# Kernel optimization log

Measured on AMD Instinct MI355X. Metric: run time of the kernel, lower is better.

Reference implementation:

```python
import jax, jax.numpy as jnp
import numpy as np

N, D, C, T, E = 8192, 512, 4, 8, 32768
H = D  # hidden_nf == input_nf == output_nf (required by the module's own shapes)


def _silu(x):
    return x * jax.nn.sigmoid(x)


def _lin(x, W, b):
    # torch Linear convention: W is [out, in]
    y = jnp.einsum('...i,oi->...o', x, W)
    return y + b


def setup_inputs() -> dict:
    key = jax.random.key(0)
    ks = jax.random.split(key, 20)
    s = 0.05  # keep activations in a sane range through stacked SiLU MLPs
    return {
        'h': jax.random.normal(ks[0], (N, D), jnp.float32),
        'coord': jax.random.normal(ks[1], (N, C, 3), jnp.float32),
        'edge_attr': jax.random.normal(ks[2], (T, E, 1), jnp.float32),
        'edge_index': jax.random.randint(ks[3], (T, 2, E), 0, N),
        'mW1': jax.random.normal(ks[4], (H, 2 * D + C * C + 1), jnp.float32) * s,
        'mb1': jnp.zeros((H,), jnp.float32),
        'mW2': jax.random.normal(ks[5], (H, H), jnp.float32) * s,
        'mb2': jnp.zeros((H,), jnp.float32),
        'nW1': jax.random.normal(ks[6], (H, H + D), jnp.float32) * s,
        'nb1': jnp.zeros((H,), jnp.float32),
        'nW2': jax.random.normal(ks[7], (D, H), jnp.float32) * s,
        'nb2': jnp.zeros((D,), jnp.float32),
        'eW1': jax.random.normal(ks[8], (H, H + 1 + H), jnp.float32) * s,
        'eb1': jnp.zeros((H,), jnp.float32),
        'eW2': jax.random.normal(ks[9], (1, H), jnp.float32) * s,
        'eb2': jnp.zeros((1,), jnp.float32),
        'relW': jax.random.normal(ks[10], (T, D, H), jnp.float32) * s,
        'cW1': jax.random.normal(ks[11], (T, H, H), jnp.float32) * s,
        'cb1': jnp.zeros((T, H), jnp.float32),
        'cW2': jax.random.normal(ks[12], (T, C, H), jnp.float32) * (s * 0.001),  # xavier gain=0.001
    }


def reference(h, coord, edge_attr, edge_index, mW1, mb1, mW2, mb2,
              nW1, nb1, nW2, nb2, eW1, eb1, eW2, eb2, relW, cW1, cb1, cW2):
    n, d = h.shape
    t, _, e = edge_index.shape
    c = coord.shape[1]
    row = edge_index[:, 0]  # [T,E]
    col = edge_index[:, 1]

    # coord2radial (per type, vectorized over type axis)
    cd = coord[row] - coord[col]                              # [T,E,C,3]
    radial = jnp.einsum('teca,teda->tecd', cd, cd)            # [T,E,C,C]
    # F.normalize(radial, dim=0): L2-normalize across the edge axis of each type
    nrm = jnp.sqrt(jnp.sum(radial * radial, axis=1, keepdims=True))
    radial = radial / jnp.maximum(nrm, 1e-12)

    # message_model (dropout = identity in eval)
    feat = jnp.concatenate([h[row], h[col], radial.reshape(t, e, c * c), edge_attr], axis=-1)
    msg = _silu(_lin(_silu(_lin(feat, mW1, mb1)), mW2, mb2))  # [T,E,H]

    # node_model: per-type segment_sum -> per-type relation linear -> sum
    seg = jax.vmap(lambda dta, ids: jax.ops.segment_sum(dta, ids, num_segments=n))(msg, row)  # [T,N,H]
    agg = jnp.einsum('tnh,tdh->nd', seg, relW)                # sum over types
    h_new = h + _lin(_silu(_lin(jnp.concatenate([h, agg], axis=-1), nW1, nb1)), nW2, nb2)

    # coord_model: per-type coord MLP weights, segment-mean over all types' edges
    hid = _silu(jnp.einsum('teh,tgh->teg', msg, cW1) + cb1[:, None, :])
    w = jnp.einsum('teg,tcg->tec', hid, cW2)                  # [T,E,C]
    trans = cd * w[..., None]                                 # [T,E,C,3]
    rows_flat = row.reshape(-1)
    sumv = jax.ops.segment_sum(trans.reshape(t * e, c, 3), rows_flat, num_segments=n)
    cnt = jax.ops.segment_sum(jnp.ones((t * e,), trans.dtype), rows_flat, num_segments=n)
    x_new = coord + sumv / jnp.maximum(cnt, 1.0)[:, None, None]

    # edge_model (note: forward passes edge_attr here, not the messages)
    ef = jnp.concatenate([h_new[row], edge_attr, h_new[col]], axis=-1)  # [T,E,H+1+H]
    m = _lin(_silu(_lin(ef, eW1, eb1)), eW2, eb2)             # [T,E,1]

    return (h_new, x_new, m)
```

## Files before the change

### kernel.cpp

```cpp
#include <hip/hip_runtime.h>
#include <cstdint>

#define NN 8192
#define DD 512
#define CC 4
#define TT 8
#define EE 32768
#define TE (TT*EE)

typedef __attribute__((ext_vector_type(8))) short short8v;
typedef __attribute__((ext_vector_type(4))) float f32x4;
typedef unsigned int uint;

constexpr int FLAG_SILU = 1, FLAG_RES = 2, FLAG_WEPI = 4, FLAG_BIAS_T = 8;

__device__ __forceinline__ float silu_f(float x) { return x / (1.f + __expf(-x)); }

__device__ __forceinline__ unsigned short f2bf(float f) {
  uint u = __builtin_bit_cast(uint, f);
  u += 0x7fffu + ((u >> 16) & 1u);
  return (unsigned short)(u >> 16);
}
__device__ __forceinline__ float bf2f(unsigned short b) {
  uint u = ((uint)b) << 16;
  return __builtin_bit_cast(float, u);
}
__device__ __forceinline__ float bflo(uint u) { return __builtin_bit_cast(float, u << 16); }
__device__ __forceinline__ float bfhi(uint u) { return __builtin_bit_cast(float, u & 0xffff0000u); }
__device__ __forceinline__ uint packbf(float a, float b) {
  return (uint)f2bf(a) | ((uint)f2bf(b) << 16);
}

__device__ __forceinline__ float wave_sum(float v) {
#pragma unroll
  for (int off = 32; off; off >>= 1) v += __shfl_xor(v, off);
  return v;
}

__device__ __forceinline__ void gload16(const void* g, void* l) {
  __builtin_amdgcn_global_load_lds(
      (const __attribute__((address_space(1))) void*)g,
      (__attribute__((address_space(3))) void*)l, 16, 0, 0);
}

__device__ __forceinline__ int xcd_swz(int i, int nwg) {
  return (i & 7) * (nwg >> 3) + (i >> 3);
}

struct AgDirect { const unsigned short* p; int K;
  __device__ const void* ptr(int m, int k, int) const { return p + (size_t)m * K + k; } };

struct AgHcat { const unsigned short* hb; const unsigned short* ab;
  __device__ const void* ptr(int m, int k, int) const {
    return (k < 512) ? (const void*)(hb + ((size_t)m << 9) + k)
                     : (const void*)(ab + ((size_t)m << 9) + (k - 512)); } };

struct AgSegG { const unsigned short* seg;
  __device__ const void* ptr(int m, int k, int) const {
    return seg + (((size_t)(k >> 9) * NN + m) << 9) + (k & 511); } };

struct BgDirect { const unsigned short* p; int K;
  __device__ const void* ptr(int o, int k, int) const { return p + (size_t)o * K + k; } };

struct BgRelG { const unsigned short* w;
  __device__ const void* ptr(int o, int k, int) const {
    return w + (((size_t)(k >> 9) * 512 + o) << 9) + (k & 511); } };

struct BgPerT { const unsigned short* w;
  __device__ const void* ptr(int o, int k, int tt) const {
    return w + (((size_t)tt << 18) + ((size_t)o << 9)) + k; } };

template<class AG, class BG>
__global__ __launch_bounds__(256)
void mgemm_k(AG ag, BG bg, int K, int tbase, int lognx,
             const float* __restrict__ bias, const float* __restrict__ res,
             float* __restrict__ outF, unsigned short* __restrict__ outB, int ldo, int flags,
             const float* __restrict__ cw2, float* __restrict__ wpart, int wstride)
{
  __shared__ __align__(16) unsigned short SM[128 * 136];
  unsigned short* As = SM;
  unsigned short* Bs = SM + 128 * 64;
  const int nwg = gridDim.x;
  const int swz = xcd_swz(blockIdx.x, nwg);
  const int xb = swz & ((1 << lognx) - 1), yb = swz >> lognx;
  const int m0 = yb * 128, o0 = xb * 128;
  const int tt = tbase + (m0 >> 15);
  const int tid = threadIdx.x, wave = tid >> 6, lane = tid & 63;
  const int wr = (wave >> 1) * 64, wc = (wave & 1) * 64;
  const int rs = lane >> 3, sl = lane & 7;

  f32x4 acc[4][4];
#pragma unroll
  for (int i = 0; i < 4; ++i)
#pragma unroll
    for (int j = 0; j < 4; ++j) acc[i][j] = (f32x4)0.f;

  for (int k0 = 0; k0 < K; k0 += 64) {
#pragma unroll
    for (int i = 0; i < 4; ++i) {
      int r = i * 32 + wave * 8 + rs;
      int slot = sl ^ (r & 7);
      gload16(ag.ptr(m0 + r, k0 + slot * 8, tt), &As[(i * 32 + wave * 8) * 64]);
    }
#pragma unroll
    for (int i = 0; i < 4; ++i) {
      int r = i * 32 + wave * 8 + rs;
      int slot = sl ^ (r & 7);
      gload16(bg.ptr(o0 + r, k0 + slot * 8, tt), &Bs[(i * 32 + wave * 8) * 64]);
    }
    __syncthreads();

    short8v a[4][2], b[4][2];
#pragma unroll
    for (int mi = 0; mi < 4; ++mi)
#pragma unroll
      for (int s = 0; s < 2; ++s) {
        int row = wr + mi * 16 + (lane & 15);
        int slot = (s * 4 + (lane >> 4)) ^ (row & 7);
        a[mi][s] = *(const short8v*)&As[row * 64 + slot * 8];
      }
#pragma unroll
    for (int ni = 0; ni < 4; ++ni)
#pragma unroll
      for (int s = 0; s < 2; ++s) {
        int row = wc + ni * 16 + (lane & 15);
        int slot = (s * 4 + (lane >> 4)) ^ (row & 7);
        b[ni][s] = *(const short8v*)&Bs[row * 64 + slot * 8];
      }
#pragma unroll
    for (int s = 0; s < 2; ++s)
#pragma unroll
      for (int mi = 0; mi < 4; ++mi)
#pragma unroll
        for (int ni = 0; ni < 4; ++ni)
          acc[mi][ni] = __builtin_amdgcn_mfma_f32_16x16x32_bf16(a[mi][s], b[ni][s], acc[mi][ni], 0, 0, 0);
    __syncthreads();
  }

  const int r4 = (lane >> 4) * 4, cl = lane & 15;
  if (flags & FLAG_WEPI) {
    const int slice = xb * 2 + (wave & 1);
    const float* cw2t = cw2 + tt * 2048;
    const float* bt = bias + tt * 512;
#pragma unroll
    for (int mi = 0; mi < 4; ++mi) {
      float sc[4][4];
#pragma unroll
      for (int rg = 0; rg < 4; ++rg)
#pragma unroll
        for (int c = 0; c < 4; ++c) sc[rg][c] = 0.f;
#pragma unroll
      for (int ni = 0; ni < 4; ++ni) {
        int col = o0 + wc + ni * 16 + cl;
        float c0 = cw2t[col], c1 = cw2t[512 + col], c2 = cw2t[1024 + col], c3 = cw2t[1536 + col];
        float bb = bt[col];
#pragma unroll
        for (int rg = 0; rg < 4; ++rg) {
          float v = silu_f(acc[mi][ni][rg] + bb);
          sc[rg][0] += v * c0; sc[rg][1] += v * c1; sc[rg][2] += v * c2; sc[rg][3] += v * c3;
        }
      }
#pragma unroll
      for (int rg = 0; rg < 4; ++rg)
#pragma unroll
        for (int c = 0; c < 4; ++c) {
          float s = sc[rg][c];
          s += __shfl_xor(s, 1); s += __shfl_xor(s, 2);
          s += __shfl_xor(s, 4); s += __shfl_xor(s, 8);
          sc[rg][c] = s;
        }
      if (cl == 0) {
        int p = m0 + wr + mi * 16 + r4;
#pragma unroll
        for (int rg = 0; rg < 4; ++rg) {
          float4 o = make_float4(sc[rg][0], sc[rg][1], sc[rg][2], sc[rg][3]);
          *(float4*)&wpart[(((size_t)slice * wstride) + p + rg) * 4] = o;
        }
      }
    }
    return;
  }
  if (outB && !outF) {
    unsigned short* Ep = SM;
#pragma unroll
    for (int mi = 0; mi < 4; ++mi)
#pragma unroll
      for (int ni = 0; ni < 4; ++ni)
#pragma unroll
        for (int rg = 0; rg < 4; ++rg) {
          int row = wr + mi * 16 + r4 + rg;
          int col = wc + ni * 16 + cl;
          float v = acc[mi][ni][rg];
          if (bias) v += (flags & FLAG_BIAS_T) ? bias[tt * 512 + o0 + col] : bias[o0 + col];
          if (flags & FLAG_SILU) v = silu_f(v);
          Ep[row * 136 + col] = f2bf(v);
        }
    __syncthreads();
#pragma unroll
    for (int p = 0; p < 8; ++p) {
      int idx = p * 256 + tid;
      int row = idx >> 4, ch = idx & 15;
      short8v vv = *(const short8v*)&Ep[row * 136 + ch * 8];
      *(short8v*)(outB + (size_t)(m0 + row) * ldo + o0 + ch * 8) = vv;
    }
    return;
  }
#pragma unroll
  for (int mi = 0; mi < 4; ++mi)
#pragma unroll
    for (int ni = 0; ni < 4; ++ni)
#pragma unroll
      for (int rg = 0; rg < 4; ++rg) {
        int row = m0 + wr + mi * 16 + r4 + rg;
        int col = o0 + wc + ni * 16 + cl;
        float v = acc[mi][ni][rg];
        if (bias) v += (flags & FLAG_BIAS_T) ? bias[tt * 512 + col] : bias[col];
        if (flags & FLAG_SILU) v = silu_f(v);
        if (flags & FLAG_RES) v += res[(size_t)row * ldo + col];
        if (outF) outF[(size_t)row * ldo + col] = v;
        if (outB) outB[(size_t)row * ldo + col] = f2bf(v);
      }
}

__global__ __launch_bounds__(256)
void cvt_k(const float* __restrict__ in, unsigned short* __restrict__ out, int n) {
  int i = blockIdx.x * 256 + threadIdx.x;
  if (i < n) out[i] = f2bf(in[i]);
}

__global__ __launch_bounds__(256)
void slicew_k(const float* __restrict__ w, unsigned short* __restrict__ o, int Kin, int col0) {
  int i = blockIdx.x * 256 + threadIdx.x;
  int r = i >> 9, k = i & 511;
  o[i] = f2bf(w[(size_t)r * Kin + col0 + k]);
}

__global__ __launch_bounds__(256)
void tailw_k(const float* __restrict__ mW1, unsigned short* __restrict__ o) {
  int i = blockIdx.x * 256 + threadIdx.x;
  if (i >= 17 * 512) return;
  int j = i >> 9, c = i & 511;
  o[i] = f2bf(mW1[(size_t)c * 1041 + 1024 + j]);
}

__global__ __launch_bounds__(256)
void weaw_k(const float* __restrict__ eW1, float* __restrict__ wea) {
  int i = blockIdx.x * 256 + threadIdx.x;
  if (i < 512) wea[i] = eW1[(size_t)i * 1025 + 512];
}

__global__ __launch_bounds__(256)
void biasb_k(const float* __restrict__ mb1, const float* __restrict__ eb1,
             float* __restrict__ pqb, float* __restrict__ ggb) {
  int i = blockIdx.x * 256 + threadIdx.x;
  if (i < 1024) {
    pqb[i] = (i < 512) ? mb1[i] : 0.f;
    ggb[i] = (i < 512) ? eb1[i] : 0.f;
  }
}

__global__ __launch_bounds__(256)
void hist_k(const int* __restrict__ eidx, int* __restrict__ deg) {
  int id = blockIdx.x * 256 + threadIdx.x;
  int t = id >> 15, e = id & (EE - 1);
  atomicAdd(&deg[(t << 13) + eidx[(t << 16) + e]], 1);
}

__global__ __launch_bounds__(256)
void scan_k(const int* __restrict__ deg, int* __restrict__ off, int* __restrict__ cursor) {
  int t = blockIdx.x, tid = threadIdx.x;
  __shared__ int lds[256];
  int base = 0;
  for (int ch = 0; ch < 32; ++ch) {
    int i = ch * 256 + tid;
    int v = deg[(t << 13) + i];
    __syncthreads();
    lds[tid] = v;
    __syncthreads();
    for (int s = 1; s < 256; s <<= 1) {
      int x = (tid >= s) ? lds[tid - s] : 0;
      __syncthreads();
      if (tid >= s) lds[tid] += x;
      __syncthreads();
    }
    int excl = base + lds[tid] - v;
    off[(t << 13) + i] = excl;
    cursor[(t << 13) + i] = excl;
    base += lds[255];
  }
}

__global__ __launch_bounds__(256)
void scat_k(const int* __restrict__ eidx, const float* __restrict__ ea, int* __restrict__ cursor,
            int* __restrict__ order, int* __restrict__ rank,
            int* __restrict__ rowS, int* __restrict__ colS, float* __restrict__ eaS) {
  int id = blockIdx.x * 256 + threadIdx.x;
  int t = id >> 15, e = id & (EE - 1);
  int r = eidx[(t << 16) + e], c = eidx[(t << 16) + EE + e];
  int pos = atomicAdd(&cursor[(t << 13) + r], 1);
  size_t g = ((size_t)t << 15) + pos;
  order[g] = e; rank[id] = pos; rowS[g] = r; colS[g] = c; eaS[g] = ea[id];
}

__global__ __launch_bounds__(256)
void cdrad_k(const float* __restrict__ coord, const int* __restrict__ eidx,
             const int* __restrict__ rank,
             float* __restrict__ cd, float* __restrict__ radial, float* __restrict__ pnrm)
{
  int m = blockIdx.x * 256 + threadIdx.x;
  int t = m >> 15, e = m & (EE - 1);
  int r = eidx[(t << 16) + e], c = eidx[(t << 16) + EE + e];
  size_t s = ((size_t)t << 15) + rank[m];
  const float4* cv4 = (const float4*)coord;
  float4 A0 = cv4[r * 3], A1 = cv4[r * 3 + 1], A2 = cv4[r * 3 + 2];
  float4 B0 = cv4[c * 3], B1 = cv4[c * 3 + 1], B2 = cv4[c * 3 + 2];
  float d[12] = {A0.x-B0.x, A0.y-B0.y, A0.z-B0.z, A0.w-B0.w,
                 A1.x-B1.x, A1.y-B1.y, A1.z-B1.z, A1.w-B1.w,
                 A2.x-B2.x, A2.y-B2.y, A2.z-B2.z, A2.w-B2.w};
  float4* cdv = (float4*)cd;
  cdv[s*3+0] = make_float4(d[0],d[1],d[2],d[3]);
  cdv[s*3+1] = make_float4(d[4],d[5],d[6],d[7]);
  cdv[s*3+2] = make_float4(d[8],d[9],d[10],d[11]);
  float rad[16], sq[16];
#pragma unroll
  for (int ci = 0; ci < 4; ++ci)
#pragma unroll
    for (int di = 0; di < 4; ++di) {
      float v = d[ci*3]*d[di*3] + d[ci*3+1]*d[di*3+1] + d[ci*3+2]*d[di*3+2];
      rad[ci*4+di] = v; sq[ci*4+di] = v * v;
    }
  float4* rv = (float4*)radial;
#pragma unroll
  for (int i = 0; i < 4; ++i)
    rv[s*4+i] = make_float4(rad[i*4], rad[i*4+1], rad[i*4+2], rad[i*4+3]);
#pragma unroll
  for (int i = 0; i < 16; ++i) sq[i] = wave_sum(sq[i]);
  __shared__ float red[4][16];
  int wv = threadIdx.x >> 6, lane = threadIdx.x & 63;
  if (lane == 0) {
#pragma unroll
    for (int i = 0; i < 16; ++i) red[wv][i] = sq[i];
  }
  __syncthreads();
  if (threadIdx.x < 16)
    pnrm[blockIdx.x * 16 + threadIdx.x] =
        red[0][threadIdx.x] + red[1][threadIdx.x] + red[2][threadIdx.x] + red[3][threadIdx.x];
}

__global__ __launch_bounds__(128)
void nrmred_k(const float* __restrict__ pnrm, float* __restrict__ nrm) {
  int t = threadIdx.x >> 4, j = threadIdx.x & 15;
  float s = 0.f;
  for (int b = 0; b < 128; ++b) s += pnrm[((t * 128 + b) << 4) + j];
  nrm[(t << 4) + j] = s;
}

__global__ __launch_bounds__(256)
void tails_k(const float* __restrict__ radial, const float* __restrict__ nrm,
             const float* __restrict__ eaS, unsigned short* __restrict__ tailm)
{
  int m = blockIdx.x * 256 + threadIdx.x;
  int t = m >> 15;
  unsigned short tmp[24];
#pragma unroll
  for (int j = 0; j < 16; ++j) {
    float r = radial[(size_t)m * 16 + j] / fmaxf(sqrtf(nrm[(t << 4) + j]), 1e-12f);
    tmp[j] = f2bf(r);
  }
  tmp[16] = f2bf(eaS[m]);
#pragma unroll
  for (int j = 17; j < 24; ++j) tmp[j] = 0;
  uint4* dst = (uint4*)(tailm + (size_t)m * 24);
  dst[0] = ((const uint4*)tmp)[0];
  dst[1] = ((const uint4*)tmp)[1];
  dst[2] = ((const uint4*)tmp)[2];
}

__global__ __launch_bounds__(256)
void msg1f_k(const unsigned short* __restrict__ PQ, const unsigned short* __restrict__ Wt,
             const unsigned short* __restrict__ tailm_g,
             const int* __restrict__ rowS_g, const int* __restrict__ colS_g,
             unsigned short* __restrict__ out)
{
  int tid = threadIdx.x;
  int e0 = xcd_swz(blockIdx.x, gridDim.x) * 16;
  uint wreg[17];
#pragma unroll
  for (int j = 0; j < 17; ++j) wreg[j] = *(const uint*)(Wt + j * 512 + tid * 2);
  for (int i = 0; i < 16; ++i) {
    int p = e0 + i;
    int r = rowS_g[p], c = colS_g[p];
    uint pv = *(const uint*)(PQ + ((size_t)r << 10) + tid * 2);
    uint qv = *(const uint*)(PQ + ((size_t)c << 10) + 512 + tid * 2);
    uint4 t0 = *(const uint4*)(tailm_g + (size_t)p * 24);
    uint4 t1 = *(const uint4*)(tailm_g + (size_t)p * 24 + 8);
    uint  t2 = *(const uint*)(tailm_g + (size_t)p * 24 + 16);
    float tl[17] = {bflo(t0.x), bfhi(t0.x), bflo(t0.y), bfhi(t0.y),
                    bflo(t0.z), bfhi(t0.z), bflo(t0.w), bfhi(t0.w),
                    bflo(t1.x), bfhi(t1.x), bflo(t1.y), bfhi(t1.y),
                    bflo(t1.z), bfhi(t1.z), bflo(t1.w), bfhi(t1.w),
                    bflo(t2)};
    float s0 = bflo(pv) + bflo(qv);
    float s1 = bfhi(pv) + bfhi(qv);
#pragma unroll
    for (int j = 0; j < 17; ++j) {
      s0 += tl[j] * bflo(wreg[j]); s1 += tl[j] * bfhi(wreg[j]);
    }
    *(uint*)(out + ((size_t)p << 9) + tid * 2) = packbf(silu_f(s0), silu_f(s1));
  }
}

__global__ __launch_bounds__(256)
void gsum_k(const unsigned short* __restrict__ msg, const int* __restrict__ offb,
            const int* __restrict__ deg, int tbase, unsigned short* __restrict__ segt)
{
  int l = xcd_swz(blockIdx.x, gridDim.x);
  int tloc = l >> 13, n = l & (NN - 1), tid = threadIdx.x;
  int t = tbase + tloc;
  int start = offb[(t << 13) + n], d = deg[(t << 13) + n];
  float s0 = 0.f, s1 = 0.f;
  const unsigned short* base = msg + (((size_t)tloc << 15) << 9);
  for (int j = 0; j < d; ++j) {
    uint v = *(const uint*)(base + ((size_t)(start + j) << 9) + tid * 2);
    s0 += bflo(v); s1 += bfhi(v);
  }
  *(uint*)(segt + (((size_t)tloc * NN + n) << 9) + tid * 2) = packbf(s0, s1);
}

__global__ __launch_bounds__(256)
void wsum_k(const float* __restrict__ wpart, float* __restrict__ wsum_out, int wstride) {
  int id = xcd_swz(blockIdx.x, gridDim.x) * 256 + threadIdx.x;
  float4 a = (float4){0.f, 0.f, 0.f, 0.f};
#pragma unroll
  for (int s = 0; s < 8; ++s) {
    float4 v = *(const float4*)&wpart[(((size_t)s * wstride) + id) * 4];
    a.x += v.x; a.y += v.y; a.z += v.z; a.w += v.w;
  }
  *(float4*)&wsum_out[(size_t)id * 4] = a;
}

__global__ __launch_bounds__(256)
void trxn_k(const float* __restrict__ coord, const float* __restrict__ cd,
            const float* __restrict__ wsum, const int* __restrict__ offb,
            const int* __restrict__ deg, float* __restrict__ xout)
{
  int id = blockIdx.x * 256 + threadIdx.x;
  int n = id / 12, j = id - n * 12, ci = j / 3;
  float s = 0.f; int cnt = 0;
#pragma unroll
  for (int t = 0; t < 8; ++t) {
    int o = offb[(t << 13) + n], d = deg[(t << 13) + n];
    size_t p = ((size_t)t << 15) + o;
    for (int k = 0; k < d; ++k)
      s += cd[(p + k) * 12 + j] * wsum[(p + k) * 4 + ci];
    cnt += d;
  }
  xout[id] = coord[id] + s / fmaxf((float)cnt, 1.f);
}

__global__ __launch_bounds__(256)
void mout_k(const unsigned short* __restrict__ GG,
            const float* __restrict__ eW2, const float* __restrict__ wea,
            const float* __restrict__ eb2, const float* __restrict__ eaS,
            const int* __restrict__ rowS, const int* __restrict__ colS,
            const int* __restrict__ order, float* __restrict__ out_m)
{
  int wid = blockIdx.x * 4 + (threadIdx.x >> 6);
  int lane = threadIdx.x & 63;
  int t = wid >> 15;
  int r = rowS[wid], c = colS[wid];
  float eav = eaS[wid];
  short8v gv  = *(const short8v*)(GG + ((size_t)r << 10) + lane * 8);
  short8v gcv = *(const short8v*)(GG + ((size_t)c << 10) + 512 + lane * 8);
  const float4* w4 = (const float4*)(eW2 + lane * 8);
  const float4* a4 = (const float4*)(wea + lane * 8);
  float4 w0 = w4[0], w1 = w4[1], a0 = a4[0], a1 = a4[1];
  float wv8[8] = {w0.x,w0.y,w0.z,w0.w,w1.x,w1.y,w1.z,w1.w};
  float av8[8] = {a0.x,a0.y,a0.z,a0.w,a1.x,a1.y,a1.z,a1.w};
  float s = 0.f;
#pragma unroll
  for (int j = 0; j < 8; ++j)
    s += wv8[j] * silu_f(bf2f((unsigned short)gv[j]) + bf2f((unsigned short)gcv[j]) + eav * av8[j]);
  s = wave_sum(s);
  if (lane == 0) out_m[((size_t)t << 15) + order[wid]] = s + eb2[0];
}

extern "C" void kernel_launch(void* const* d_in, const int* in_sizes, int n_in,
                              void* d_out, int out_size, void* d_ws, size_t ws_size,
                              hipStream_t stream)
{
  const float* h     = (const float*)d_in[0];
  const float* coord = (const float*)d_in[1];
  const float* ea    = (const float*)d_in[2];
  const int*   eidx  = (const int*)  d_in[3];
  const float* mW1   = (const float*)d_in[4];
  const float* mb1   = (const float*)d_in[5];
  const float* mW2   = (const float*)d_in[6];
  const float* mb2   = (const float*)d_in[7];
  const float* nW1   = (const float*)d_in[8];
  const float* nb1   = (const float*)d_in[9];
  const float* nW2   = (const float*)d_in[10];
  const float* nb2   = (const float*)d_in[11];
  const float* eW1   = (const float*)d_in[12];
  const float* eb1   = (const float*)d_in[13];
  const float* eW2   = (const float*)d_in[14];
  const float* eb2   = (const float*)d_in[15];
  const float* relW  = (const float*)d_in[16];
  const float* cW1   = (const float*)d_in[17];
  const float* cb1   = (const float*)d_in[18];
  const float* cW2   = (const float*)d_in[19];

  float* out   = (float*)d_out;
  float* out_h = out;
  float* out_x = out + (size_t)NN * DD;
  float* out_m = out_x + (size_t)NN * CC * 3;

  char* ws = (char*)d_ws;
  size_t off = 0;
  auto alloc = [&](size_t bytes) -> void* {
    void* p = ws + off; off += (bytes + 255) & ~(size_t)255; return p;
  };
  float* cd     = (float*)alloc((size_t)TE * 12 * 4);
  unsigned short* tailm = (unsigned short*)alloc((size_t)TE * 24 * 2);
  float* agg    = (float*)alloc((size_t)NN * 512 * 4);
  unsigned short* h_bf  = (unsigned short*)alloc((size_t)NN * 512 * 2);
  unsigned short* hn_bf = (unsigned short*)alloc((size_t)NN * 512 * 2);
  unsigned short* PQb   = (unsigned short*)alloc((size_t)NN * 1024 * 2);
  unsigned short* GGb   = PQb;
  unsigned short* mW1pq = (unsigned short*)alloc((size_t)1024 * 512 * 2);
  unsigned short* mW1t  = (unsigned short*)alloc((size_t)17 * 512 * 2);
  unsigned short* mW2b  = (unsigned short*)alloc((size_t)512 * 512 * 2);
  unsigned short* nW1b  = (unsigned short*)alloc((size_t)512 * 1024 * 2);
  unsigned short* nW2b  = (unsigned short*)alloc((size_t)512 * 512 * 2);
  unsigned short* eGc   = (unsigned short*)alloc((size_t)1024 * 512 * 2);
  float* weab   = (float*)alloc(512 * 4);
  float* pqbias = (float*)alloc(1024 * 4);
  float* ggbias = (float*)alloc(1024 * 4);
  unsigned short* relWb = (unsigned short*)alloc((size_t)TT * 512 * 512 * 2);
  unsigned short* cW1b  = (unsigned short*)alloc((size_t)TT * 512 * 512 * 2);
  int* deg     = (int*)alloc((size_t)TT * NN * 4);
  int* offb    = (int*)alloc((size_t)TT * NN * 4);
  int* cursor  = (int*)alloc((size_t)TT * NN * 4);
  int* order   = (int*)alloc((size_t)TE * 4);
  int* rank    = (int*)alloc((size_t)TE * 4);
  int* rowS    = (int*)alloc((size_t)TE * 4);
  int* colS    = (int*)alloc((size_t)TE * 4);
  float* eaS   = (float*)alloc((size_t)TE * 4);
  float* wsumb = (float*)alloc((size_t)TE * 4 * 4);
  float* pnrm  = (float*)alloc((size_t)(TE / 256) * 16 * 4);
  float* nrm   = (float*)alloc((size_t)TT * 16 * 4);

  const size_t perG = (size_t)EE * 512 * 2 * 2 + (size_t)NN * 512 * 2 + (size_t)8 * EE * 16;
  int G = 4;
  while (G > 1 && off + (size_t)G * perG + (1 << 20) > ws_size) G >>= 1;
  unsigned short* bufA = (unsigned short*)alloc((size_t)G * EE * 512 * 2);
  unsigned short* bufB = (unsigned short*)alloc((size_t)G * EE * 512 * 2);
  unsigned short* segt = (unsigned short*)alloc((size_t)G * NN * 512 * 2);
  float* wpart = (float*)alloc((size_t)8 * G * EE * 4 * 4);
  unsigned short* aggb = segt;
  float* radial = (float*)bufA;

  hipMemsetAsync(deg, 0, (size_t)TT * NN * 4, stream);
  hipMemsetAsync(agg, 0, (size_t)NN * 512 * 4, stream);

  auto cvt = [&](const float* in, unsigned short* o, int n) {
    cvt_k<<<(n + 255) / 256, 256, 0, stream>>>(in, o, n);
  };
  cvt(h,    h_bf,  NN * 512);
  cvt(mW2,  mW2b,  512 * 512);
  cvt(nW1,  nW1b,  512 * 1024);
  cvt(nW2,  nW2b,  512 * 512);
  cvt(relW, relWb, TT * 512 * 512);
  cvt(cW1,  cW1b,  TT * 512 * 512);
  slicew_k<<<1024, 256, 0, stream>>>(mW1, mW1pq, 1041, 0);
  slicew_k<<<1024, 256, 0, stream>>>(mW1, mW1pq + 512 * 512, 1041, 512);
  tailw_k<<<34, 256, 0, stream>>>(mW1, mW1t);
  slicew_k<<<1024, 256, 0, stream>>>(eW1, eGc, 1025, 0);
  slicew_k<<<1024, 256, 0, stream>>>(eW1, eGc + 512 * 512, 1025, 513);
  weaw_k<<<2, 256, 0, stream>>>(eW1, weab);
  biasb_k<<<4, 256, 0, stream>>>(mb1, eb1, pqbias, ggbias);

  hist_k<<<TE / 256, 256, 0, stream>>>(eidx, deg);
  scan_k<<<TT, 256, 0, stream>>>(deg, offb, cursor);
  scat_k<<<TE / 256, 256, 0, stream>>>(eidx, ea, cursor, order, rank, rowS, colS, eaS);
  cdrad_k<<<TE / 256, 256, 0, stream>>>(coord, eidx, rank, cd, radial, pnrm);
  nrmred_k<<<1, 128, 0, stream>>>(pnrm, nrm);
  tails_k<<<TE / 256, 256, 0, stream>>>(radial, nrm, eaS, tailm);

  mgemm_k<<<512, 256, 0, stream>>>(AgDirect{h_bf, 512}, BgDirect{mW1pq, 512}, 512, 0, 3,
      pqbias, nullptr, nullptr, PQb, 1024, 0, nullptr, nullptr, 0);

  for (int g = 0; g < TT / G; ++g) {
    const int tbase = g * G;
    const size_t gb = (size_t)tbase << 15;
    msg1f_k<<<(G * EE) / 16, 256, 0, stream>>>(PQb, mW1t, tailm + gb * 24,
        rowS + gb, colS + gb, bufA);
    mgemm_k<<<4 * (G * EE / 128), 256, 0, stream>>>(AgDirect{bufA, 512},
        BgDirect{mW2b, 512}, 512, tbase, 2,
        mb2, nullptr, nullptr, bufB, 512, FLAG_SILU, nullptr, nullptr, 0);
    gsum_k<<<G * NN, 256, 0, stream>>>(bufB, offb, deg, tbase, segt);
    mgemm_k<<<4 * (NN / 128), 256, 0, stream>>>(AgSegG{segt},
        BgRelG{relWb + ((size_t)tbase << 18)}, G * 512, 0, 2,
        nullptr, agg, agg, nullptr, 512, FLAG_RES, nullptr, nullptr, 0);
    mgemm_k<<<4 * (G * EE / 128), 256, 0, stream>>>(AgDirect{bufB, 512},
        BgPerT{cW1b}, 512, tbase, 2,
        cb1, nullptr, nullptr, nullptr, 512, FLAG_SILU | FLAG_WEPI | FLAG_BIAS_T,
        cW2, wpart, G * EE);
    wsum_k<<<(G * EE) / 256, 256, 0, stream>>>(wpart, wsumb + gb * 4, G * EE);
  }

  trxn_k<<<(NN * 12) / 256, 256, 0, stream>>>(coord, cd, wsumb, offb, deg, out_x);

  cvt(agg, aggb, NN * 512);
  mgemm_k<<<4 * (NN / 128), 256, 0, stream>>>(AgHcat{h_bf, aggb}, BgDirect{nW1b, 1024}, 1024, 0, 2,
      nb1, nullptr, nullptr, bufA, 512, FLAG_SILU, nullptr, nullptr, 0);
  mgemm_k<<<4 * (NN / 128), 256, 0, stream>>>(AgDirect{bufA, 512}, BgDirect{nW2b, 512}, 512, 0, 2,
      nb2, h, out_h, hn_bf, 512, FLAG_RES, nullptr, nullptr, 0);

  mgemm_k<<<512, 256, 0, stream>>>(AgDirect{hn_bf, 512}, BgDirect{eGc, 512}, 512, 0, 3,
      ggbias, nullptr, nullptr, GGb, 1024, 0, nullptr, nullptr, 0);
  mout_k<<<TE / 4, 256, 0, stream>>>(GGb, eW2, weab, eb2, eaS, rowS, colS, order, out_m);

  (void)in_sizes; (void)n_in; (void)out_size; (void)ws_size;
}
```

Before: 1.433 ms.

## Add 256-row 512-thread GEMM for edge MLPs, fuse converts and scatter kernels

```diff
diff --git a/kernel.cpp b/kernel.cpp
--- a/kernel.cpp
+++ b/kernel.cpp
@@ -74,14 +74,12 @@
 __global__ __launch_bounds__(256)
 void mgemm_k(AG ag, BG bg, int K, int tbase, int lognx,
              const float* __restrict__ bias, const float* __restrict__ res,
-             float* __restrict__ outF, unsigned short* __restrict__ outB, int ldo, int flags,
-             const float* __restrict__ cw2, float* __restrict__ wpart, int wstride)
+             float* __restrict__ outF, unsigned short* __restrict__ outB, int ldo, int flags)
 {
   __shared__ __align__(16) unsigned short SM[128 * 136];
   unsigned short* As = SM;
   unsigned short* Bs = SM + 128 * 64;
-  const int nwg = gridDim.x;
-  const int swz = xcd_swz(blockIdx.x, nwg);
+  const int swz = xcd_swz(blockIdx.x, gridDim.x);
   const int xb = swz & ((1 << lognx) - 1), yb = swz >> lognx;
   const int m0 = yb * 128, o0 = xb * 128;
   const int tt = tbase + (m0 >> 15);
@@ -109,7 +107,6 @@
       gload16(bg.ptr(o0 + r, k0 + slot * 8, tt), &Bs[(i * 32 + wave * 8) * 64]);
     }
     __syncthreads();
-
     short8v a[4][2], b[4][2];
 #pragma unroll
     for (int mi = 0; mi < 4; ++mi)
@@ -138,48 +135,6 @@
   }
 
   const int r4 = (lane >> 4) * 4, cl = lane & 15;
-  if (flags & FLAG_WEPI) {
-    const int slice = xb * 2 + (wave & 1);
-    const float* cw2t = cw2 + tt * 2048;
-    const float* bt = bias + tt * 512;
-#pragma unroll
-    for (int mi = 0; mi < 4; ++mi) {
-      float sc[4][4];
-#pragma unroll
-      for (int rg = 0; rg < 4; ++rg)
-#pragma unroll
-        for (int c = 0; c < 4; ++c) sc[rg][c] = 0.f;
-#pragma unroll
-      for (int ni = 0; ni < 4; ++ni) {
-        int col = o0 + wc + ni * 16 + cl;
-        float c0 = cw2t[col], c1 = cw2t[512 + col], c2 = cw2t[1024 + col], c3 = cw2t[1536 + col];
-        float bb = bt[col];
-#pragma unroll
-        for (int rg = 0; rg < 4; ++rg) {
-          float v = silu_f(acc[mi][ni][rg] + bb);
-          sc[rg][0] += v * c0; sc[rg][1] += v * c1; sc[rg][2] += v * c2; sc[rg][3] += v * c3;
-        }
-      }
-#pragma unroll
-      for (int rg = 0; rg < 4; ++rg)
-#pragma unroll
-        for (int c = 0; c < 4; ++c) {
-          float s = sc[rg][c];
-          s += __shfl_xor(s, 1); s += __shfl_xor(s, 2);
-          s += __shfl_xor(s, 4); s += __shfl_xor(s, 8);
-          sc[rg][c] = s;
-        }
-      if (cl == 0) {
-        int p = m0 + wr + mi * 16 + r4;
-#pragma unroll
-        for (int rg = 0; rg < 4; ++rg) {
-          float4 o = make_float4(sc[rg][0], sc[rg][1], sc[rg][2], sc[rg][3]);
-          *(float4*)&wpart[(((size_t)slice * wstride) + p + rg) * 4] = o;
-        }
-      }
-    }
-    return;
-  }
   if (outB && !outF) {
     unsigned short* Ep = SM;
 #pragma unroll
@@ -222,6 +177,164 @@
       }
 }
 
+template<class AG, class BG>
+__global__ __launch_bounds__(512)
+void mgemm2_k(AG ag, BG bg, int K, int tbase,
+              const float* __restrict__ bias,
+              unsigned short* __restrict__ outB, int flags,
+              const float* __restrict__ cw2, float* __restrict__ wpart, int wstride)
+{
+  __shared__ __align__(16) unsigned short SM[(256 + 128) * 64];
+  unsigned short* As = SM;
+  unsigned short* Bs = SM + 256 * 64;
+  const int swz = xcd_swz(blockIdx.x, gridDim.x);
+  const int xb = swz & 3, yb = swz >> 2;
+  const int m0 = yb * 256, o0 = xb * 128;
+  const int tt = tbase + (m0 >> 15);
+  const int tid = threadIdx.x, wave = tid >> 6, lane = tid & 63;
+  const int wr = (wave >> 1) * 64, wc = (wave & 1) * 64;
+  const int rs = lane >> 3, sl = lane & 7;
+
+  f32x4 acc[4][4];
+#pragma unroll
+  for (int i = 0; i < 4; ++i)
+#pragma unroll
+    for (int j = 0; j < 4; ++j) acc[i][j] = (f32x4)0.f;
+
+  for (int k0 = 0; k0 < K; k0 += 64) {
+#pragma unroll
+    for (int i = 0; i < 4; ++i) {
+      int r = i * 64 + wave * 8 + rs;
+      int slot = sl ^ (r & 7);
+      gload16(ag.ptr(m0 + r, k0 + slot * 8, tt), &As[(i * 64 + wave * 8) * 64]);
+    }
+#pragma unroll
+    for (int i = 0; i < 2; ++i) {
+      int r = i * 64 + wave * 8 + rs;
+      int slot = sl ^ (r & 7);
+      gload16(bg.ptr(o0 + r, k0 + slot * 8, tt), &Bs[(i * 64 + wave * 8) * 64]);
+    }
+    __syncthreads();
+    short8v a[4][2], b[4][2];
+#pragma unroll
+    for (int mi = 0; mi < 4; ++mi)
+#pragma unroll
+      for (int s = 0; s < 2; ++s) {
+        int row = wr + mi * 16 + (lane & 15);
+        int slot = (s * 4 + (lane >> 4)) ^ (row & 7);
+        a[mi][s] = *(const short8v*)&As[row * 64 + slot * 8];
+      }
+#pragma unroll
+    for (int ni = 0; ni < 4; ++ni)
+#pragma unroll
+      for (int s = 0; s < 2; ++s) {
+        int row = wc + ni * 16 + (lane & 15);
+        int slot = (s * 4 + (lane >> 4)) ^ (row & 7);
+        b[ni][s] = *(const short8v*)&Bs[row * 64 + slot * 8];
+      }
+#pragma unroll
+    for (int s = 0; s < 2; ++s)
+#pragma unroll
+      for (int mi = 0; mi < 4; ++mi)
+#pragma unroll
+        for (int ni = 0; ni < 4; ++ni)
+          acc[mi][ni] = __builtin_amdgcn_mfma_f32_16x16x32_bf16(a[mi][s], b[ni][s], acc[mi][ni], 0, 0, 0);
+    __syncthreads();
+  }
+
+  const int r4 = (lane >> 4) * 4, cl = lane & 15;
+  if (flags & FLAG_WEPI) {
+    const int slice = xb * 2 + (wave & 1);
+    const float* cw2t = cw2 + tt * 2048;
+    const float* bt = bias + tt * 512;
+#pragma unroll
+    for (int mi = 0; mi < 4; ++mi) {
+      float sc[4][4];
+#pragma unroll
+      for (int rg = 0; rg < 4; ++rg)
+#pragma unroll
+        for (int c = 0; c < 4; ++c) sc[rg][c] = 0.f;
+#pragma unroll
+      for (int ni = 0; ni < 4; ++ni) {
+        int col = o0 + wc + ni * 16 + cl;
+        float c0 = cw2t[col], c1 = cw2t[512 + col], c2 = cw2t[1024 + col], c3 = cw2t[1536 + col];
+        float bb = bt[col];
+#pragma unroll
+        for (int rg = 0; rg < 4; ++rg) {
+          float v = silu_f(acc[mi][ni][rg] + bb);
+          sc[rg][0] += v * c0; sc[rg][1] += v * c1; sc[rg][2] += v * c2; sc[rg][3] += v * c3;
+        }
+      }
+#pragma unroll
+      for (int rg = 0; rg < 4; ++rg)
+#pragma unroll
+        for (int c = 0; c < 4; ++c) {
+          float s = sc[rg][c];
+          s += __shfl_xor(s, 1); s += __shfl_xor(s, 2);
+          s += __shfl_xor(s, 4); s += __shfl_xor(s, 8);
+          sc[rg][c] = s;
+        }
+      if (cl == 0) {
+        int p = m0 + wr + mi * 16 + r4;
+#pragma unroll
+        for (int rg = 0; rg < 4; ++rg) {
+          float4 o = make_float4(sc[rg][0], sc[rg][1], sc[rg][2], sc[rg][3]);
+          *(float4*)&wpart[(((size_t)slice * wstride) + p + rg) * 4] = o;
+        }
+      }
+    }
+    return;
+  }
+  unsigned short* Ep = SM;
+#pragma unroll
+  for (int hh = 0; hh < 2; ++hh) {
+    if ((wr >> 7) == hh) {
+#pragma unroll
+      for (int mi = 0; mi < 4; ++mi)
+#pragma unroll
+        for (int ni = 0; ni < 4; ++ni)
+#pragma unroll
+          for (int rg = 0; rg < 4; ++rg) {
+            int row = (wr & 127) + mi * 16 + r4 + rg;
+            int col = wc + ni * 16 + cl;
+            float v = acc[mi][ni][rg];
+            v += bias[o0 + col];
+            if (flags & FLAG_SILU) v = silu_f(v);
+            Ep[row * 136 + col] = f2bf(v);
+          }
+    }
+    __syncthreads();
+#pragma unroll
+    for (int p = 0; p < 4; ++p) {
+      int idx = p * 512 + tid;
+      int row = idx >> 4, ch = idx & 15;
+      short8v vv = *(const short8v*)&Ep[row * 136 + ch * 8];
+      *(short8v*)(outB + (size_t)(m0 + hh * 128 + row) * 512 + o0 + ch * 8) = vv;
+    }
+    __syncthreads();
+  }
+}
+
+__global__ __launch_bounds__(256)
+void cvtall_k(const float* h, const float* mW2, const float* nW1, const float* nW2,
+              const float* relW, const float* cW1,
+              unsigned short* hb, unsigned short* mW2b, unsigned short* nW1b,
+              unsigned short* nW2b, unsigned short* relWb, unsigned short* cW1b)
+{
+  int i = blockIdx.x * 256 + threadIdx.x;
+  if (i < 4194304) { hb[i] = f2bf(h[i]); return; }
+  i -= 4194304;
+  if (i < 262144) { mW2b[i] = f2bf(mW2[i]); return; }
+  i -= 262144;
+  if (i < 524288) { nW1b[i] = f2bf(nW1[i]); return; }
+  i -= 524288;
+  if (i < 262144) { nW2b[i] = f2bf(nW2[i]); return; }
+  i -= 262144;
+  if (i < 2097152) { relWb[i] = f2bf(relW[i]); return; }
+  i -= 2097152;
+  cW1b[i] = f2bf(cW1[i]);
+}
+
 __global__ __launch_bounds__(256)
 void cvt_k(const float* __restrict__ in, unsigned short* __restrict__ out, int n) {
   int i = blockIdx.x * 256 + threadIdx.x;
@@ -291,26 +404,18 @@
 }
 
 __global__ __launch_bounds__(256)
-void scat_k(const int* __restrict__ eidx, const float* __restrict__ ea, int* __restrict__ cursor,
-            int* __restrict__ order, int* __restrict__ rank,
-            int* __restrict__ rowS, int* __restrict__ colS, float* __restrict__ eaS) {
-  int id = blockIdx.x * 256 + threadIdx.x;
-  int t = id >> 15, e = id & (EE - 1);
-  int r = eidx[(t << 16) + e], c = eidx[(t << 16) + EE + e];
-  int pos = atomicAdd(&cursor[(t << 13) + r], 1);
-  size_t g = ((size_t)t << 15) + pos;
-  order[g] = e; rank[id] = pos; rowS[g] = r; colS[g] = c; eaS[g] = ea[id];
-}
-
-__global__ __launch_bounds__(256)
-void cdrad_k(const float* __restrict__ coord, const int* __restrict__ eidx,
-             const int* __restrict__ rank,
-             float* __restrict__ cd, float* __restrict__ radial, float* __restrict__ pnrm)
+void scatcd_k(const int* __restrict__ eidx, const float* __restrict__ ea,
+              const float* __restrict__ coord, int* __restrict__ cursor,
+              int* __restrict__ order, int* __restrict__ rowS, int* __restrict__ colS,
+              float* __restrict__ eaS, float* __restrict__ cd,
+              float* __restrict__ radial, float* __restrict__ pnrm)
 {
   int m = blockIdx.x * 256 + threadIdx.x;
   int t = m >> 15, e = m & (EE - 1);
   int r = eidx[(t << 16) + e], c = eidx[(t << 16) + EE + e];
-  size_t s = ((size_t)t << 15) + rank[m];
+  int pos = atomicAdd(&cursor[(t << 13) + r], 1);
+  size_t s = ((size_t)t << 15) + pos;
+  order[s] = e; rowS[s] = r; colS[s] = c; eaS[s] = ea[m];
   const float4* cv4 = (const float4*)coord;
   float4 A0 = cv4[r * 3], A1 = cv4[r * 3 + 1], A2 = cv4[r * 3 + 2];
   float4 B0 = cv4[c * 3], B1 = cv4[c * 3 + 1], B2 = cv4[c * 3 + 2];
@@ -465,7 +570,7 @@
             const int* __restrict__ rowS, const int* __restrict__ colS,
             const int* __restrict__ order, float* __restrict__ out_m)
 {
-  int wid = blockIdx.x * 4 + (threadIdx.x >> 6);
+  int wid = xcd_swz(blockIdx.x, gridDim.x) * 4 + (threadIdx.x >> 6);
   int lane = threadIdx.x & 63;
   int t = wid >> 15;
   int r = rowS[wid], c = colS[wid];
@@ -542,7 +647,6 @@
   int* offb    = (int*)alloc((size_t)TT * NN * 4);
   int* cursor  = (int*)alloc((size_t)TT * NN * 4);
   int* order   = (int*)alloc((size_t)TE * 4);
-  int* rank    = (int*)alloc((size_t)TE * 4);
   int* rowS    = (int*)alloc((size_t)TE * 4);
   int* colS    = (int*)alloc((size_t)TE * 4);
   float* eaS   = (float*)alloc((size_t)TE * 4);
@@ -563,15 +667,8 @@
   hipMemsetAsync(deg, 0, (size_t)TT * NN * 4, stream);
   hipMemsetAsync(agg, 0, (size_t)NN * 512 * 4, stream);
 
-  auto cvt = [&](const float* in, unsigned short* o, int n) {
-    cvt_k<<<(n + 255) / 256, 256, 0, stream>>>(in, o, n);
-  };
-  cvt(h,    h_bf,  NN * 512);
-  cvt(mW2,  mW2b,  512 * 512);
-  cvt(nW1,  nW1b,  512 * 1024);
-  cvt(nW2,  nW2b,  512 * 512);
-  cvt(relW, relWb, TT * 512 * 512);
-  cvt(cW1,  cW1b,  TT * 512 * 512);
+  cvtall_k<<<9437184 / 256, 256, 0, stream>>>(h, mW2, nW1, nW2, relW, cW1,
+      h_bf, mW2b, nW1b, nW2b, relWb, cW1b);
   slicew_k<<<1024, 256, 0, stream>>>(mW1, mW1pq, 1041, 0);
   slicew_k<<<1024, 256, 0, stream>>>(mW1, mW1pq + 512 * 512, 1041, 512);
   tailw_k<<<34, 256, 0, stream>>>(mW1, mW1t);
@@ -582,43 +679,42 @@
 
   hist_k<<<TE / 256, 256, 0, stream>>>(eidx, deg);
   scan_k<<<TT, 256, 0, stream>>>(deg, offb, cursor);
-  scat_k<<<TE / 256, 256, 0, stream>>>(eidx, ea, cursor, order, rank, rowS, colS, eaS);
-  cdrad_k<<<TE / 256, 256, 0, stream>>>(coord, eidx, rank, cd, radial, pnrm);
+  scatcd_k<<<TE / 256, 256, 0, stream>>>(eidx, ea, coord, cursor,
+      order, rowS, colS, eaS, cd, radial, pnrm);
   nrmred_k<<<1, 128, 0, stream>>>(pnrm, nrm);
   tails_k<<<TE / 256, 256, 0, stream>>>(radial, nrm, eaS, tailm);
 
   mgemm_k<<<512, 256, 0, stream>>>(AgDirect{h_bf, 512}, BgDirect{mW1pq, 512}, 512, 0, 3,
-      pqbias, nullptr, nullptr, PQb, 1024, 0, nullptr, nullptr, 0);
+      pqbias, nullptr, nullptr, PQb, 1024, 0);
 
   for (int g = 0; g < TT / G; ++g) {
     const int tbase = g * G;
     const size_t gb = (size_t)tbase << 15;
     msg1f_k<<<(G * EE) / 16, 256, 0, stream>>>(PQb, mW1t, tailm + gb * 24,
         rowS + gb, colS + gb, bufA);
-    mgemm_k<<<4 * (G * EE / 128), 256, 0, stream>>>(AgDirect{bufA, 512},
-        BgDirect{mW2b, 512}, 512, tbase, 2,
-        mb2, nullptr, nullptr, bufB, 512, FLAG_SILU, nullptr, nullptr, 0);
+    mgemm2_k<<<4 * (G * EE / 256), 512, 0, stream>>>(AgDirect{bufA, 512},
+        BgDirect{mW2b, 512}, 512, tbase,
+        mb2, bufB, FLAG_SILU, nullptr, nullptr, 0);
     gsum_k<<<G * NN, 256, 0, stream>>>(bufB, offb, deg, tbase, segt);
     mgemm_k<<<4 * (NN / 128), 256, 0, stream>>>(AgSegG{segt},
         BgRelG{relWb + ((size_t)tbase << 18)}, G * 512, 0, 2,
-        nullptr, agg, agg, nullptr, 512, FLAG_RES, nullptr, nullptr, 0);
-    mgemm_k<<<4 * (G * EE / 128), 256, 0, stream>>>(AgDirect{bufB, 512},
-        BgPerT{cW1b}, 512, tbase, 2,
-        cb1, nullptr, nullptr, nullptr, 512, FLAG_SILU | FLAG_WEPI | FLAG_BIAS_T,
-        cW2, wpart, G * EE);
+        nullptr, agg, agg, nullptr, 512, FLAG_RES);
+    mgemm2_k<<<4 * (G * EE / 256), 512, 0, stream>>>(AgDirect{bufB, 512},
+        BgPerT{cW1b}, 512, tbase,
+        cb1, nullptr, FLAG_SILU | FLAG_WEPI | FLAG_BIAS_T, cW2, wpart, G * EE);
     wsum_k<<<(G * EE) / 256, 256, 0, stream>>>(wpart, wsumb + gb * 4, G * EE);
   }
 
   trxn_k<<<(NN * 12) / 256, 256, 0, stream>>>(coord, cd, wsumb, offb, deg, out_x);
 
-  cvt(agg, aggb, NN * 512);
+  cvt_k<<<(NN * 512) / 256, 256, 0, stream>>>(agg, aggb, NN * 512);
   mgemm_k<<<4 * (NN / 128), 256, 0, stream>>>(AgHcat{h_bf, aggb}, BgDirect{nW1b, 1024}, 1024, 0, 2,
-      nb1, nullptr, nullptr, bufA, 512, FLAG_SILU, nullptr, nullptr, 0);
+      nb1, nullptr, nullptr, bufA, 512, FLAG_SILU);
   mgemm_k<<<4 * (NN / 128), 256, 0, stream>>>(AgDirect{bufA, 512}, BgDirect{nW2b, 512}, 512, 0, 2,
-      nb2, h, out_h, hn_bf, 512, FLAG_RES, nullptr, nullptr, 0);
+      nb2, h, out_h, hn_bf, 512, FLAG_RES);
 
   mgemm_k<<<512, 256, 0, stream>>>(AgDirect{hn_bf, 512}, BgDirect{eGc, 512}, 512, 0, 3,
-      ggbias, nullptr, nullptr, GGb, 1024, 0, nullptr, nullptr, 0);
+      ggbias, nullptr, nullptr, GGb, 1024, 0);
   mout_k<<<TE / 4, 256, 0, stream>>>(GGb, eW2, weab, eb2, eaS, rowS, colS, order, out_m);
 
   (void)in_sizes; (void)n_in; (void)out_size; (void)ws_size;
```

New measurement: 1.405 ms. -2.0%, faster.
